# Kernel tuning notes

Hardware: AMD Instinct MI355X
Metric: run time of the kernel (lower is better)

The kernel has to match this reference:

```python
import jax, jax.numpy as jnp
import numpy as np

D_MODEL, HEADS, D_FF = 1024, 16, 4096
D_K = D_MODEL // HEADS
EPS = 1e-5


def layer_norm(x, g, b):
    mu = jnp.mean(x, axis=-1, keepdims=True)
    var = jnp.mean((x - mu) ** 2, axis=-1, keepdims=True)
    return (x - mu) * jax.lax.rsqrt(var + EPS) * g + b


def setup_inputs() -> dict:
    key = jax.random.key(0)
    ks = jax.random.split(key, 16)
    B, S = 2, 2048
    s = 0.02
    return {
        "src": jax.random.normal(ks[0], (B, S, D_MODEL), jnp.float32),
        "corr": jax.random.normal(ks[1], (B, S, S), jnp.float32),
        "pos": jax.random.normal(ks[2], (B, S, D_MODEL), jnp.float32),
        "Wq": jax.random.normal(ks[3], (D_MODEL, D_MODEL), jnp.float32) * s,
        "bq": jnp.zeros((D_MODEL,), jnp.float32),
        "Wk": jax.random.normal(ks[4], (D_MODEL, D_MODEL), jnp.float32) * s,
        "bk": jnp.zeros((D_MODEL,), jnp.float32),
        "Wv": jax.random.normal(ks[5], (D_MODEL, D_MODEL), jnp.float32) * s,
        "bv": jnp.zeros((D_MODEL,), jnp.float32),
        "Wo": jax.random.normal(ks[6], (D_MODEL, D_MODEL), jnp.float32) * s,
        "bo": jnp.zeros((D_MODEL,), jnp.float32),
        "W1": jax.random.normal(ks[7], (D_MODEL, D_FF), jnp.float32) * s,
        "b1": jnp.zeros((D_FF,), jnp.float32),
        "W2": jax.random.normal(ks[8], (D_FF, D_MODEL), jnp.float32) * s,
        "b2": jnp.zeros((D_MODEL,), jnp.float32),
        "g1": jnp.ones((D_MODEL,), jnp.float32),
        "be1": jnp.zeros((D_MODEL,), jnp.float32),
        "g2": jnp.ones((D_MODEL,), jnp.float32),
        "be2": jnp.zeros((D_MODEL,), jnp.float32),
    }


def reference(src, corr, pos, Wq, bq, Wk, bk, Wv, bv, Wo, bo, W1, b1, W2, b2, g1, be1, g2, be2):
    B, S, _ = src.shape
    qk_in = src + pos  # with_pos_embed for q and k; value uses raw src
    # QKV projections -> [B, H, S, d_k]
    def split_heads(x):
        return x.reshape(B, S, HEADS, D_K).transpose(0, 2, 1, 3)
    q = split_heads(qk_in @ Wq + bq)
    k = split_heads(qk_in @ Wk + bk)
    v = split_heads(src @ Wv + bv)
    # scores [B, H, S, S] with additive correlation bias before softmax
    scores = jnp.einsum("bhqd,bhkd->bhqk", q, k) / jnp.sqrt(jnp.float32(D_K))
    scores = scores + corr[:, None, :, :]
    attn = jax.nn.softmax(scores, axis=-1)
    ctx = jnp.einsum("bhqk,bhkd->bhqd", attn, v)
    concat = ctx.transpose(0, 2, 1, 3).reshape(B, S, D_MODEL)
    attn_out = concat @ Wo + bo
    # post-norm residual blocks (dropout = identity in eval)
    x = layer_norm(src + attn_out, g1, be1)
    ffn = jax.nn.relu(x @ W1 + b1) @ W2 + b2
    x = layer_norm(x + ffn, g2, be2)
    return x
```

## Files before the change

### kernel.cpp

```cpp
#include <hip/hip_runtime.h>
#include <hip/hip_bf16.h>

#define S_LEN  2048
#define BATCH  2
#define DMODEL 1024
#define NHEAD  16
#define DHEAD  64
#define DFF    4096
#define NTOK   (BATCH * S_LEN)
#define QKVLD  3072
#define NSPLIT 2

typedef __attribute__((ext_vector_type(8))) short short8;
typedef __attribute__((ext_vector_type(4))) short short4v;
typedef __attribute__((ext_vector_type(4))) float f32x4;

__device__ __forceinline__ short f2bs(float f) {
  __hip_bfloat16 h = __float2bfloat16(f);
  short s;
  __builtin_memcpy(&s, &h, sizeof(short));
  return s;
}

__device__ __forceinline__ float bs2f(short s) {
  unsigned u = ((unsigned)(unsigned short)s) << 16;
  float f;
  __builtin_memcpy(&f, &u, sizeof(float));
  return f;
}

__device__ __forceinline__ f32x4 mfma16(short8 a, short8 b, f32x4 c) {
  return __builtin_amdgcn_mfma_f32_16x16x32_bf16(a, b, c, 0, 0, 0);
}

__device__ __forceinline__ void load_lds16(const short* g, short* l) {
  __builtin_amdgcn_global_load_lds(
      (const __attribute__((address_space(1))) void*)g,
      (__attribute__((address_space(3))) void*)l, 16, 0, 0);
}

__global__ void prep_static(
    const float* __restrict__ Wq, const float* __restrict__ Wk,
    const float* __restrict__ Wv, const float* __restrict__ Wo,
    const float* __restrict__ W1, const float* __restrict__ W2,
    const float* __restrict__ bq, const float* __restrict__ bk,
    const float* __restrict__ bv,
    short* __restrict__ WqkvT, short* __restrict__ WoT,
    short* __restrict__ W1T, short* __restrict__ W2T,
    float* __restrict__ bqkv) {
  const int gid = blockIdx.x;
  const int tx = threadIdx.x, ty = threadIdx.y;

  if (gid >= 12288) {
    const int i = (gid - 12288) * 256 + ty * 32 + tx;
    float v;
    if (i < DMODEL) v = bq[i] * 0.125f;
    else if (i < 2 * DMODEL) v = bk[i - DMODEL];
    else v = bv[i - 2 * DMODEL];
    bqkv[i] = v;
    return;
  }

  const float* in;
  short* out;
  int R, C, t;
  float scale = 1.0f;
  if (gid < 4096) {
    t = gid & 1023;
    R = C = 1024;
    if (gid < 1024)      { in = Wq; out = WqkvT;                 scale = 0.125f; }
    else if (gid < 2048) { in = Wk; out = WqkvT + 1024 * 1024; }
    else if (gid < 3072) { in = Wv; out = WqkvT + 2 * 1024 * 1024; }
    else                 { in = Wo; out = WoT; }
  } else if (gid < 8192) {
    t = gid - 4096; in = W1; out = W1T; R = 1024; C = 4096;
  } else {
    t = gid - 8192; in = W2; out = W2T; R = 4096; C = 1024;
  }
  const int tpr = C >> 5;
  const int c0 = (t % tpr) * 32, r0 = (t / tpr) * 32;

  __shared__ float tile[32][33];
#pragma unroll
  for (int i = 0; i < 32; i += 8)
    tile[ty + i][tx] = in[(size_t)(r0 + ty + i) * C + c0 + tx];
  __syncthreads();
#pragma unroll
  for (int i = 0; i < 32; i += 8)
    out[(size_t)(c0 + ty + i) * R + r0 + tx] = f2bs(tile[tx][ty + i] * scale);
}

__global__ void prep_inputs(const float* __restrict__ src, const float* __restrict__ pos,
                            const float* __restrict__ corr,
                            short* __restrict__ qkb, short* __restrict__ srcb,
                            short* __restrict__ corrb) {
  const int gid = blockIdx.x;
  if (gid < 4096) {
    const int i = gid * 1024 + threadIdx.x * 4;
    float4 s = *(const float4*)(src + i);
    float4 p = *(const float4*)(pos + i);
    short4v q4 = {f2bs(s.x + p.x), f2bs(s.y + p.y), f2bs(s.z + p.z), f2bs(s.w + p.w)};
    short4v s4 = {f2bs(s.x), f2bs(s.y), f2bs(s.z), f2bs(s.w)};
    *(short4v*)(qkb + i) = q4;
    *(short4v*)(srcb + i) = s4;
  } else {
    const size_t i = ((size_t)(gid - 4096)) * 1024 + threadIdx.x * 4;
    float4 c = *(const float4*)(corr + i);
    short4v o = {f2bs(c.x), f2bs(c.y), f2bs(c.z), f2bs(c.w)};
    *(short4v*)(corrb + i) = o;
  }
}

__global__ __launch_bounds__(256) void transpose_bf16(
    const short* __restrict__ in, short* __restrict__ out, int R, int LDin) {
  __shared__ __attribute__((aligned(16))) short tile[64][72];
  const int c0 = blockIdx.x * 64, r0 = blockIdx.y * 64;
#pragma unroll
  for (int i = 0; i < 2; i++) {
    const int idx = threadIdx.x + 256 * i;
    const int rr = idx >> 3, cc8 = (idx & 7) * 8;
    *(int4*)(&tile[rr][cc8]) = *(const int4*)(in + (size_t)(r0 + rr) * LDin + c0 + cc8);
  }
  __syncthreads();
#pragma unroll
  for (int i = 0; i < 2; i++) {
    const int idx = threadIdx.x + 256 * i;
    const int rr = idx >> 3, cc8 = (idx & 7) * 8;
    short8 v;
#pragma unroll
    for (int j = 0; j < 8; j++) v[j] = tile[cc8 + j][rr];
    *(short8*)(out + (size_t)(c0 + rr) * R + r0 + cc8) = v;
  }
}

template <int RELU, int OUT_BF16>
__global__ __launch_bounds__(256) void gemm_bt(
    const short* __restrict__ A0, const short* __restrict__ A1,
    const short* __restrict__ Bt, const float* __restrict__ bias,
    float* __restrict__ Cf, short* __restrict__ Cb,
    int M, int N, int K, int splitcol) {
  __shared__ __attribute__((aligned(16))) short As[128 * 32];
  __shared__ __attribute__((aligned(16))) short Bs[128 * 32];

  const int tid = threadIdx.x;
  const int wave = tid >> 6, lane = tid & 63;
  const int lm = lane & 15, lq = lane >> 4;
  const int row0 = blockIdx.y * 128, col0 = blockIdx.x * 128;
  const int wr = (wave >> 1) * 64, wc = (wave & 1) * 64;

  const short* A = (col0 < splitcol) ? A0 : A1;
  const short* ag = A + (size_t)(row0 + wave * 32 + (lane >> 2)) * K + (lane & 3) * 8;
  const short* bg = Bt + (size_t)(col0 + wave * 32 + (lane >> 2)) * K + (lane & 3) * 8;
  short* asl = &As[wave * 32 * 32];
  short* bsl = &Bs[wave * 32 * 32];

  f32x4 acc[4][4];
#pragma unroll
  for (int i = 0; i < 4; i++)
#pragma unroll
    for (int j = 0; j < 4; j++) acc[i][j] = (f32x4){0.f, 0.f, 0.f, 0.f};

  for (int k0 = 0; k0 < K; k0 += 32) {
    load_lds16(ag + k0, asl);
    load_lds16(ag + (size_t)16 * K + k0, asl + 16 * 32);
    load_lds16(bg + k0, bsl);
    load_lds16(bg + (size_t)16 * K + k0, bsl + 16 * 32);
    __syncthreads();

    short8 af[4], bfr[4];
#pragma unroll
    for (int i = 0; i < 4; i++)
      af[i] = *(const short8*)(&As[(wr + 16 * i + lm) * 32 + lq * 8]);
#pragma unroll
    for (int j = 0; j < 4; j++)
      bfr[j] = *(const short8*)(&Bs[(wc + 16 * j + lm) * 32 + lq * 8]);
#pragma unroll
    for (int i = 0; i < 4; i++)
#pragma unroll
      for (int j = 0; j < 4; j++) acc[i][j] = mfma16(af[i], bfr[j], acc[i][j]);
    __syncthreads();
  }

#pragma unroll
  for (int i = 0; i < 4; i++) {
#pragma unroll
    for (int j = 0; j < 4; j++) {
      const int col = col0 + wc + 16 * j + lm;
      const float bs = bias[col];
#pragma unroll
      for (int r = 0; r < 4; r++) {
        const int row = row0 + wr + 16 * i + lq * 4 + r;
        float v = acc[i][j][r] + bs;
        if (RELU) v = fmaxf(v, 0.f);
        if (OUT_BF16)
          Cb[(size_t)row * N + col] = f2bs(v);
        else
          Cf[(size_t)row * N + col] = v;
      }
    }
  }
}

__global__ __launch_bounds__(256) void gemm_bt_part(
    const short* __restrict__ A, const short* __restrict__ Bt,
    float* __restrict__ Cf, int M, int N, int K, int Kslice) {
  __shared__ __attribute__((aligned(16))) short As[128 * 32];
  __shared__ __attribute__((aligned(16))) short Bs[128 * 32];

  const int tid = threadIdx.x;
  const int wave = tid >> 6, lane = tid & 63;
  const int lm = lane & 15, lq = lane >> 4;
  const int row0 = blockIdx.y * 128, col0 = blockIdx.x * 128;
  const int kbase = blockIdx.z * Kslice;
  const int wr = (wave >> 1) * 64, wc = (wave & 1) * 64;
  Cf += (size_t)blockIdx.z * M * N;

  const short* ag = A + (size_t)(row0 + wave * 32 + (lane >> 2)) * K + (lane & 3) * 8;
  const short* bg = Bt + (size_t)(col0 + wave * 32 + (lane >> 2)) * K + (lane & 3) * 8;
  short* asl = &As[wave * 32 * 32];
  short* bsl = &Bs[wave * 32 * 32];

  f32x4 acc[4][4];
#pragma unroll
  for (int i = 0; i < 4; i++)
#pragma unroll
    for (int j = 0; j < 4; j++) acc[i][j] = (f32x4){0.f, 0.f, 0.f, 0.f};

  for (int k0 = kbase; k0 < kbase + Kslice; k0 += 32) {
    load_lds16(ag + k0, asl);
    load_lds16(ag + (size_t)16 * K + k0, asl + 16 * 32);
    load_lds16(bg + k0, bsl);
    load_lds16(bg + (size_t)16 * K + k0, bsl + 16 * 32);
    __syncthreads();

    short8 af[4], bfr[4];
#pragma unroll
    for (int i = 0; i < 4; i++)
      af[i] = *(const short8*)(&As[(wr + 16 * i + lm) * 32 + lq * 8]);
#pragma unroll
    for (int j = 0; j < 4; j++)
      bfr[j] = *(const short8*)(&Bs[(wc + 16 * j + lm) * 32 + lq * 8]);
#pragma unroll
    for (int i = 0; i < 4; i++)
#pragma unroll
      for (int j = 0; j < 4; j++) acc[i][j] = mfma16(af[i], bfr[j], acc[i][j]);
    __syncthreads();
  }

#pragma unroll
  for (int i = 0; i < 4; i++) {
#pragma unroll
    for (int j = 0; j < 4; j++) {
      const int col = col0 + wc + 16 * j + lm;
#pragma unroll
      for (int r = 0; r < 4; r++) {
        const int row = row0 + wr + 16 * i + lq * 4 + r;
        Cf[(size_t)row * N + col] = acc[i][j][r];
      }
    }
  }
}

__global__ __launch_bounds__(256, 8) void attn_kernel(
    const short* __restrict__ QKV,
    const short* __restrict__ VT,
    const short* __restrict__ corrb,
    float* __restrict__ Op,
    float* __restrict__ lp) {
  const int h = blockIdx.x, qtile = blockIdx.y;
  const int b = blockIdx.z >> 1, split = blockIdx.z & 1;
  const int koff = split * (S_LEN / NSPLIT);
  const int tid = threadIdx.x;
  const int wave = tid >> 6, lane = tid & 63;
  const int lm = lane & 15, lq = lane >> 4;
  const int qb = qtile * 64 + wave * 16;
  const int fx = lm & 7;
  const int fy = (lm >> 1) & 3;

  __shared__ __attribute__((aligned(16))) short Ks[32 * 64];
  __shared__ __attribute__((aligned(16))) short Vs[64 * 32];
  __shared__ __attribute__((aligned(16))) short Ps[4 * 16 * 32];

  const short* q0 = QKV + (size_t)(b * S_LEN + qb + lm) * QKVLD + h * DHEAD;
  const short8 qA0 = *(const short8*)(q0 + lq * 8);
  const short8 qA1 = *(const short8*)(q0 + lq * 8 + 32);

  f32x4 oA[4];
#pragma unroll
  for (int t = 0; t < 4; t++) oA[t] = (f32x4){0.f, 0.f, 0.f, 0.f};
  f32x4 lacc = (f32x4){0.f, 0.f, 0.f, 0.f};

  const short* c0 = corrb + (size_t)(b * S_LEN + qb + lm) * S_LEN;

  const int krow = tid >> 3, ku = tid & 7;
  short* kdst = &Ks[krow * 64 + ((ku ^ (krow & 7)) * 8)];
  const short* kgp = QKV + (size_t)(b * S_LEN + koff + krow) * QKVLD + DMODEL +
                     h * DHEAD + ku * 8;
  const int vrow = tid >> 2, vu = tid & 3;
  short* vdst = &Vs[vrow * 32 + ((vu ^ ((vrow >> 1) & 3)) * 8)];
  const short* vgp = VT + (size_t)(h * DHEAD + vrow) * NTOK + b * S_LEN + koff + vu * 8;

  for (int kt = koff; kt < koff + S_LEN / NSPLIT; kt += 32) {
    *(int4*)kdst = *(const int4*)kgp;
    *(int4*)vdst = *(const int4*)vgp;
    kgp += (size_t)32 * QKVLD;
    vgp += 32;
    __syncthreads();

    f32x4 sv[2];
    __builtin_amdgcn_s_setprio(1);
#pragma unroll
    for (int t = 0; t < 2; t++) {
      const int rb = (t * 16 + lm) * 64;
      const short8 kf0 = *(const short8*)(&Ks[rb + (lq ^ fx) * 8]);
      const short8 kf1 = *(const short8*)(&Ks[rb + ((lq + 4) ^ fx) * 8]);
      f32x4 a = (f32x4){0.f, 0.f, 0.f, 0.f};
      a = mfma16(kf0, qA0, a);
      a = mfma16(kf1, qA1, a);
      sv[t] = a;
    }
    __builtin_amdgcn_s_setprio(0);

#pragma unroll
    for (int t = 0; t < 2; t++) {
      const short4v cr = *(const short4v*)(c0 + kt + t * 16 + lq * 4);
#pragma unroll
      for (int r = 0; r < 4; r++)
        sv[t][r] = __expf(sv[t][r] + bs2f(cr[r]));
      lacc += sv[t];
      short4v pA = {f2bs(sv[t][0]), f2bs(sv[t][1]), f2bs(sv[t][2]), f2bs(sv[t][3])};
      const int pu = ((2 * t + (lq >> 1)) ^ fy) * 8 + (lq & 1) * 4;
      *(short4v*)(&Ps[wave * 512 + lm * 32 + pu]) = pA;
    }

    const short8 pA0 = *(const short8*)(&Ps[wave * 512 + lm * 32 + (lq ^ fy) * 8]);
    __builtin_amdgcn_s_setprio(1);
#pragma unroll
    for (int t = 0; t < 4; t++) {
      const int vrb = (t * 16 + lm) * 32;
      const short8 vf0 = *(const short8*)(&Vs[vrb + (lq ^ fy) * 8]);
      oA[t] = mfma16(vf0, pA0, oA[t]);
    }
    __builtin_amdgcn_s_setprio(0);
    __syncthreads();
  }

  float lA = lacc[0] + lacc[1] + lacc[2] + lacc[3];
  lA += __shfl_xor(lA, 16);
  lA += __shfl_xor(lA, 32);
  if (lq == 0)
    lp[((size_t)split * NTOK + b * S_LEN + qb + lm) * NHEAD + h] = lA;
  float* opA = Op + (size_t)split * NTOK * DMODEL +
               (size_t)(b * S_LEN + qb + lm) * DMODEL + h * DHEAD;
#pragma unroll
  for (int t = 0; t < 4; t++)
    *(f32x4*)(opA + t * 16 + lq * 4) = oA[t];
}

__global__ __launch_bounds__(256) void combine_ctx(
    const float* __restrict__ Op, const float* __restrict__ lp,
    short* __restrict__ ctx) {
  const size_t idx = ((size_t)blockIdx.x * 256 + threadIdx.x) * 4;
  const int token = (int)(idx >> 10);
  const int d = (int)(idx & 1023);
  const int h = d >> 6;
  f32x4 o = (f32x4){0.f, 0.f, 0.f, 0.f};
  float l = 0.f;
#pragma unroll
  for (int s = 0; s < NSPLIT; s++) {
    o += *(const f32x4*)(Op + (size_t)s * NTOK * DMODEL + idx);
    l += lp[((size_t)s * NTOK + token) * NHEAD + h];
  }
  const float inv = 1.0f / l;
  short4v ov = {f2bs(o[0] * inv), f2bs(o[1] * inv),
                f2bs(o[2] * inv), f2bs(o[3] * inv)};
  *(short4v*)(ctx + idx) = ov;
}

__global__ __launch_bounds__(256) void residual_ln3(
    const float* __restrict__ xa, const float* __restrict__ p0,
    const float* __restrict__ p1, const float* __restrict__ bias,
    const float* __restrict__ g, const float* __restrict__ be,
    float* __restrict__ outf, short* __restrict__ outb) {
  const int row = blockIdx.x;
  const int t = threadIdx.x;
  const size_t base = (size_t)row * DMODEL + t * 4;
  float4 a = *(const float4*)(xa + base);
  f32x4 q0 = *(const f32x4*)(p0 + base);
  f32x4 q1 = *(const f32x4*)(p1 + base);
  f32x4 bb = *(const f32x4*)(bias + t * 4);
  const float v0 = a.x + q0[0] + q1[0] + bb[0];
  const float v1 = a.y + q0[1] + q1[1] + bb[1];
  const float v2 = a.z + q0[2] + q1[2] + bb[2];
  const float v3 = a.w + q0[3] + q1[3] + bb[3];
  float sum = v0 + v1 + v2 + v3;
  float sq = v0 * v0 + v1 * v1 + v2 * v2 + v3 * v3;
#pragma unroll
  for (int off = 1; off < 64; off <<= 1) {
    sum += __shfl_xor(sum, off);
    sq += __shfl_xor(sq, off);
  }
  __shared__ float ssum[4], ssq[4];
  const int wave = t >> 6;
  if ((t & 63) == 0) { ssum[wave] = sum; ssq[wave] = sq; }
  __syncthreads();
  sum = ssum[0] + ssum[1] + ssum[2] + ssum[3];
  sq = ssq[0] + ssq[1] + ssq[2] + ssq[3];
  const float mean = sum * (1.0f / DMODEL);
  const float var = sq * (1.0f / DMODEL) - mean * mean;
  const float rstd = rsqrtf(var + 1e-5f);
  float4 gv = *(const float4*)(g + t * 4);
  float4 bv = *(const float4*)(be + t * 4);
  const float o0 = (v0 - mean) * rstd * gv.x + bv.x;
  const float o1 = (v1 - mean) * rstd * gv.y + bv.y;
  const float o2 = (v2 - mean) * rstd * gv.z + bv.z;
  const float o3 = (v3 - mean) * rstd * gv.w + bv.w;
  if (outf) {
    float4 ov = {o0, o1, o2, o3};
    *(float4*)(outf + base) = ov;
  }
  if (outb) {
    short4v ob = {f2bs(o0), f2bs(o1), f2bs(o2), f2bs(o3)};
    *(short4v*)(outb + base) = ob;
  }
}

extern "C" void kernel_launch(void* const* d_in, const int* in_sizes, int n_in,
                              void* d_out, int out_size, void* d_ws, size_t ws_size,
                              hipStream_t stream) {
  const float* src = (const float*)d_in[0];
  const float* corr = (const float*)d_in[1];
  const float* pos = (const float*)d_in[2];
  const float* Wq = (const float*)d_in[3];
  const float* bq = (const float*)d_in[4];
  const float* Wk = (const float*)d_in[5];
  const float* bk = (const float*)d_in[6];
  const float* Wv = (const float*)d_in[7];
  const float* bv = (const float*)d_in[8];
  const float* Wo = (const float*)d_in[9];
  const float* bo = (const float*)d_in[10];
  const float* W1 = (const float*)d_in[11];
  const float* b1 = (const float*)d_in[12];
  const float* W2 = (const float*)d_in[13];
  const float* b2 = (const float*)d_in[14];
  const float* g1 = (const float*)d_in[15];
  const float* be1 = (const float*)d_in[16];
  const float* g2 = (const float*)d_in[17];
  const float* be2 = (const float*)d_in[18];
  float* out = (float*)d_out;

  char* ws = (char*)d_ws;
  size_t off = 0;
  auto alloc = [&](size_t bytes) {
    char* p = ws + off;
    off += (bytes + 255) & ~(size_t)255;
    return p;
  };
  short* WqkvT = (short*)alloc((size_t)QKVLD * DMODEL * 2);
  short* WoT = (short*)alloc((size_t)DMODEL * DMODEL * 2);
  short* W1T = (short*)alloc((size_t)DFF * DMODEL * 2);
  short* W2T = (short*)alloc((size_t)DMODEL * DFF * 2);
  float* bqkv = (float*)alloc((size_t)QKVLD * 4);
  short* qkb = (short*)alloc((size_t)NTOK * DMODEL * 2);
  short* srcb = (short*)alloc((size_t)NTOK * DMODEL * 2);
  short* QKVb = (short*)alloc((size_t)NTOK * QKVLD * 2);
  short* VTt = (short*)alloc((size_t)DMODEL * NTOK * 2);
  short* corrb = (short*)alloc((size_t)BATCH * S_LEN * S_LEN * 2);
  short* ctxb = (short*)alloc((size_t)NTOK * DMODEL * 2);
  float* lp = (float*)alloc((size_t)NSPLIT * NTOK * NHEAD * 4);
  float* Pp = (float*)alloc((size_t)2 * NTOK * DMODEL * 4);
  short* Hb = (short*)alloc((size_t)NTOK * DFF * 2);
  float* Op = Pp;
  float* x1f = (float*)alloc((size_t)NTOK * DMODEL * 4);
  short* x1b = (short*)alloc((size_t)NTOK * DMODEL * 2);

  prep_static<<<12300, dim3(32, 8), 0, stream>>>(
      Wq, Wk, Wv, Wo, W1, W2, bq, bk, bv, WqkvT, WoT, W1T, W2T, bqkv);

  prep_inputs<<<12288, 256, 0, stream>>>(src, pos, corr, qkb, srcb, corrb);

  gemm_bt<0, 1><<<dim3(QKVLD / 128, NTOK / 128), 256, 0, stream>>>(
      qkb, srcb, WqkvT, bqkv, nullptr, QKVb, NTOK, QKVLD, DMODEL, 2048);

  transpose_bf16<<<dim3(DMODEL / 64, NTOK / 64), 256, 0, stream>>>(
      QKVb + 2048, VTt, NTOK, QKVLD);

  attn_kernel<<<dim3(NHEAD, S_LEN / 64, BATCH * NSPLIT), 256, 0, stream>>>(
      QKVb, VTt, corrb, Op, lp);
  combine_ctx<<<(NTOK * DMODEL) / (256 * 4), 256, 0, stream>>>(Op, lp, ctxb);

  gemm_bt_part<<<dim3(DMODEL / 128, NTOK / 128, 2), 256, 0, stream>>>(
      ctxb, WoT, Pp, NTOK, DMODEL, DMODEL, DMODEL / 2);

  residual_ln3<<<NTOK, 256, 0, stream>>>(src, Pp, Pp + (size_t)NTOK * DMODEL,
                                         bo, g1, be1, x1f, x1b);

  gemm_bt<1, 1><<<dim3(DFF / 128, NTOK / 128), 256, 0, stream>>>(
      x1b, x1b, W1T, b1, nullptr, Hb, NTOK, DFF, DMODEL, 1 << 30);

  gemm_bt_part<<<dim3(DMODEL / 128, NTOK / 128, 2), 256, 0, stream>>>(
      Hb, W2T, Pp, NTOK, DMODEL, DFF, DFF / 2);

  residual_ln3<<<NTOK, 256, 0, stream>>>(x1f, Pp, Pp + (size_t)NTOK * DMODEL,
                                         b2, g2, be2, out, nullptr);
}
```

Baseline: 478.2 us.

## Use 256x256 double-buffered 8-wave GEMM and 8-wave attention blocks

Replaces the 128x128 single-buffered QKV and FFN1 GEMM with a 512-thread kernel on 256x256 tiles and 64-wide K steps. It double-buffers swizzled LDS and interleaves global-to-LDS loads with MFMA phases to hide memory latency and raise data reuse. The attention kernel also grows to 8 waves covering 128 queries, with K and V staging split between the two thread halves. The cost is larger LDS use (128 KB per GEMM block), fewer GEMM blocks (e.g. 192 for QKV), and possible occupancy or tail-effect issues.

```diff
diff --git a/kernel.cpp b/kernel.cpp
--- a/kernel.cpp
+++ b/kernel.cpp
@@ -133,72 +133,154 @@
   }
 }
 
-template <int RELU, int OUT_BF16>
-__global__ __launch_bounds__(256) void gemm_bt(
+template <int RELU>
+__global__ __launch_bounds__(512, 2) void gemm_bt8(
     const short* __restrict__ A0, const short* __restrict__ A1,
     const short* __restrict__ Bt, const float* __restrict__ bias,
-    float* __restrict__ Cf, short* __restrict__ Cb,
-    int M, int N, int K, int splitcol) {
-  __shared__ __attribute__((aligned(16))) short As[128 * 32];
-  __shared__ __attribute__((aligned(16))) short Bs[128 * 32];
+    short* __restrict__ Cb, int M, int N, int K, int splitcol) {
+  __shared__ __attribute__((aligned(16))) short As[2][256 * 64];
+  __shared__ __attribute__((aligned(16))) short Bs[2][256 * 64];
 
   const int tid = threadIdx.x;
   const int wave = tid >> 6, lane = tid & 63;
   const int lm = lane & 15, lq = lane >> 4;
-  const int row0 = blockIdx.y * 128, col0 = blockIdx.x * 128;
-  const int wr = (wave >> 1) * 64, wc = (wave & 1) * 64;
-
+  const int wm = wave >> 2, wn = wave & 3;
+  const int row0 = blockIdx.y * 256, col0 = blockIdx.x * 256;
   const short* A = (col0 < splitcol) ? A0 : A1;
-  const short* ag = A + (size_t)(row0 + wave * 32 + (lane >> 2)) * K + (lane & 3) * 8;
-  const short* bg = Bt + (size_t)(col0 + wave * 32 + (lane >> 2)) * K + (lane & 3) * 8;
-  short* asl = &As[wave * 32 * 32];
-  short* bsl = &Bs[wave * 32 * 32];
-
-  f32x4 acc[4][4];
-#pragma unroll
-  for (int i = 0; i < 4; i++)
-#pragma unroll
-    for (int j = 0; j < 4; j++) acc[i][j] = (f32x4){0.f, 0.f, 0.f, 0.f};
-
-  for (int k0 = 0; k0 < K; k0 += 32) {
-    load_lds16(ag + k0, asl);
-    load_lds16(ag + (size_t)16 * K + k0, asl + 16 * 32);
-    load_lds16(bg + k0, bsl);
-    load_lds16(bg + (size_t)16 * K + k0, bsl + 16 * 32);
-    __syncthreads();
-
-    short8 af[4], bfr[4];
-#pragma unroll
-    for (int i = 0; i < 4; i++)
-      af[i] = *(const short8*)(&As[(wr + 16 * i + lm) * 32 + lq * 8]);
-#pragma unroll
-    for (int j = 0; j < 4; j++)
-      bfr[j] = *(const short8*)(&Bs[(wc + 16 * j + lm) * 32 + lq * 8]);
-#pragma unroll
-    for (int i = 0; i < 4; i++)
-#pragma unroll
-      for (int j = 0; j < 4; j++) acc[i][j] = mfma16(af[i], bfr[j], acc[i][j]);
-    __syncthreads();
-  }
-
-#pragma unroll
-  for (int i = 0; i < 4; i++) {
-#pragma unroll
-    for (int j = 0; j < 4; j++) {
-      const int col = col0 + wc + 16 * j + lm;
-      const float bs = bias[col];
-#pragma unroll
-      for (int r = 0; r < 4; r++) {
-        const int row = row0 + wr + 16 * i + lq * 4 + r;
-        float v = acc[i][j][r] + bs;
-        if (RELU) v = fmaxf(v, 0.f);
-        if (OUT_BF16)
-          Cb[(size_t)row * N + col] = f2bs(v);
-        else
-          Cf[(size_t)row * N + col] = v;
+
+  const int srow = tid >> 3;
+  const int lu = ((tid & 7) ^ (srow & 7)) * 8;
+
+#define STG(DSTHALF, SRC, LD, TR, KT) do {                                     \
+    const short* _s = (SRC) + (size_t)((TR) + srow) * (LD) +                   \
+                      (size_t)(KT) * 64 + lu;                                  \
+    load_lds16(_s, (DSTHALF) + wave * 512);                                    \
+    load_lds16(_s + (size_t)64 * (LD), (DSTHALF) + 4096 + wave * 512);         \
+  } while (0)
+
+  const int fk = lm & 7;
+  const int u0 = (lq ^ fk) * 8, u1 = ((4 + lq) ^ fk) * 8;
+  const int arow = (wm * 64 + lm) * 64;
+  const int brow = (wn * 32 + lm) * 64;
+
+  f32x4 acc[2][4][2][2];
+#pragma unroll
+  for (int a = 0; a < 2; a++)
+#pragma unroll
+    for (int i = 0; i < 4; i++)
+#pragma unroll
+      for (int b = 0; b < 2; b++)
+#pragma unroll
+        for (int j = 0; j < 2; j++) acc[a][i][b][j] = (f32x4){0.f, 0.f, 0.f, 0.f};
+
+  short8 af[4][2], bf0[2][2], bf1[2][2];
+
+  const int NT = K >> 6;
+  STG(&As[0][0],    A,  K, row0,       0);
+  STG(&Bs[0][0],    Bt, K, col0,       0);
+  STG(&As[0][8192], A,  K, row0 + 128, 0);
+  STG(&Bs[0][8192], Bt, K, col0 + 128, 0);
+  STG(&As[1][0],    A,  K, row0,       1);
+  STG(&Bs[1][0],    Bt, K, col0,       1);
+  asm volatile("s_waitcnt vmcnt(4)" ::: "memory");
+  __builtin_amdgcn_s_barrier();
+
+  for (int t = 0; t < NT; ++t) {
+    const int cur = t & 1, nxt = cur ^ 1;
+    const int t1 = (t + 1 < NT) ? t + 1 : NT - 1;
+    const int t2 = (t + 2 < NT) ? t + 2 : NT - 1;
+    const short* Ac = As[cur];
+    const short* Bc = Bs[cur];
+
+    STG(&As[nxt][8192], A, K, row0 + 128, t1);
+#pragma unroll
+    for (int i = 0; i < 4; i++) {
+      af[i][0] = *(const short8*)(&Ac[arow + i * 1024 + u0]);
+      af[i][1] = *(const short8*)(&Ac[arow + i * 1024 + u1]);
+    }
+#pragma unroll
+    for (int j = 0; j < 2; j++) {
+      bf0[j][0] = *(const short8*)(&Bc[brow + j * 1024 + u0]);
+      bf0[j][1] = *(const short8*)(&Bc[brow + j * 1024 + u1]);
+    }
+    __builtin_amdgcn_s_setprio(1);
+#pragma unroll
+    for (int i = 0; i < 4; i++)
+#pragma unroll
+      for (int j = 0; j < 2; j++) {
+        acc[0][i][0][j] = mfma16(af[i][0], bf0[j][0], acc[0][i][0][j]);
+        acc[0][i][0][j] = mfma16(af[i][1], bf0[j][1], acc[0][i][0][j]);
       }
-    }
-  }
+    __builtin_amdgcn_s_setprio(0);
+    __builtin_amdgcn_s_barrier();
+
+    STG(&Bs[nxt][8192], Bt, K, col0 + 128, t1);
+#pragma unroll
+    for (int j = 0; j < 2; j++) {
+      bf1[j][0] = *(const short8*)(&Bc[8192 + brow + j * 1024 + u0]);
+      bf1[j][1] = *(const short8*)(&Bc[8192 + brow + j * 1024 + u1]);
+    }
+    __builtin_amdgcn_s_setprio(1);
+#pragma unroll
+    for (int i = 0; i < 4; i++)
+#pragma unroll
+      for (int j = 0; j < 2; j++) {
+        acc[0][i][1][j] = mfma16(af[i][0], bf1[j][0], acc[0][i][1][j]);
+        acc[0][i][1][j] = mfma16(af[i][1], bf1[j][1], acc[0][i][1][j]);
+      }
+    __builtin_amdgcn_s_setprio(0);
+    __builtin_amdgcn_s_barrier();
+
+    STG(&As[cur][0], A, K, row0, t2);
+#pragma unroll
+    for (int i = 0; i < 4; i++) {
+      af[i][0] = *(const short8*)(&Ac[8192 + arow + i * 1024 + u0]);
+      af[i][1] = *(const short8*)(&Ac[8192 + arow + i * 1024 + u1]);
+    }
+    __builtin_amdgcn_s_setprio(1);
+#pragma unroll
+    for (int i = 0; i < 4; i++)
+#pragma unroll
+      for (int j = 0; j < 2; j++) {
+        acc[1][i][0][j] = mfma16(af[i][0], bf0[j][0], acc[1][i][0][j]);
+        acc[1][i][0][j] = mfma16(af[i][1], bf0[j][1], acc[1][i][0][j]);
+      }
+    __builtin_amdgcn_s_setprio(0);
+    __builtin_amdgcn_s_barrier();
+
+    STG(&Bs[cur][0], Bt, K, col0, t2);
+    __builtin_amdgcn_s_setprio(1);
+#pragma unroll
+    for (int i = 0; i < 4; i++)
+#pragma unroll
+      for (int j = 0; j < 2; j++) {
+        acc[1][i][1][j] = mfma16(af[i][0], bf1[j][0], acc[1][i][1][j]);
+        acc[1][i][1][j] = mfma16(af[i][1], bf1[j][1], acc[1][i][1][j]);
+      }
+    __builtin_amdgcn_s_setprio(0);
+    asm volatile("s_waitcnt vmcnt(4)" ::: "memory");
+    __builtin_amdgcn_s_barrier();
+  }
+#undef STG
+
+#pragma unroll
+  for (int a = 0; a < 2; a++)
+#pragma unroll
+    for (int i = 0; i < 4; i++)
+#pragma unroll
+      for (int b = 0; b < 2; b++)
+#pragma unroll
+        for (int j = 0; j < 2; j++) {
+          const int col = col0 + b * 128 + wn * 32 + j * 16 + lm;
+          const float bsv = bias[col];
+#pragma unroll
+          for (int r = 0; r < 4; r++) {
+            const int row = row0 + a * 128 + wm * 64 + i * 16 + lq * 4 + r;
+            float v = acc[a][i][b][j][r] + bsv;
+            if (RELU) v = fmaxf(v, 0.f);
+            Cb[(size_t)row * N + col] = f2bs(v);
+          }
+        }
 }
 
 __global__ __launch_bounds__(256) void gemm_bt_part(
@@ -261,7 +343,7 @@
   }
 }
 
-__global__ __launch_bounds__(256, 8) void attn_kernel(
+__global__ __launch_bounds__(512, 8) void attn_kernel(
     const short* __restrict__ QKV,
     const short* __restrict__ VT,
     const short* __restrict__ corrb,
@@ -273,13 +355,13 @@
   const int tid = threadIdx.x;
   const int wave = tid >> 6, lane = tid & 63;
   const int lm = lane & 15, lq = lane >> 4;
-  const int qb = qtile * 64 + wave * 16;
+  const int qb = qtile * 128 + wave * 16;
   const int fx = lm & 7;
   const int fy = (lm >> 1) & 3;
 
   __shared__ __attribute__((aligned(16))) short Ks[32 * 64];
   __shared__ __attribute__((aligned(16))) short Vs[64 * 32];
-  __shared__ __attribute__((aligned(16))) short Ps[4 * 16 * 32];
+  __shared__ __attribute__((aligned(16))) short Ps[8 * 16 * 32];
 
   const short* q0 = QKV + (size_t)(b * S_LEN + qb + lm) * QKVLD + h * DHEAD;
   const short8 qA0 = *(const short8*)(q0 + lq * 8);
@@ -292,19 +374,26 @@
 
   const short* c0 = corrb + (size_t)(b * S_LEN + qb + lm) * S_LEN;
 
-  const int krow = tid >> 3, ku = tid & 7;
-  short* kdst = &Ks[krow * 64 + ((ku ^ (krow & 7)) * 8)];
-  const short* kgp = QKV + (size_t)(b * S_LEN + koff + krow) * QKVLD + DMODEL +
-                     h * DHEAD + ku * 8;
-  const int vrow = tid >> 2, vu = tid & 3;
-  short* vdst = &Vs[vrow * 32 + ((vu ^ ((vrow >> 1) & 3)) * 8)];
-  const short* vgp = VT + (size_t)(h * DHEAD + vrow) * NTOK + b * S_LEN + koff + vu * 8;
+  const int st = tid & 255;
+  const bool isK = tid < 256;
+  short* sdst;
+  const short* sgp;
+  size_t sstep;
+  if (isK) {
+    const int krow = st >> 3, ku = st & 7;
+    sdst = &Ks[krow * 64 + ((ku ^ (krow & 7)) * 8)];
+    sgp = QKV + (size_t)(b * S_LEN + koff + krow) * QKVLD + DMODEL + h * DHEAD + ku * 8;
+    sstep = (size_t)32 * QKVLD;
+  } else {
+    const int vrow = st >> 2, vu = st & 3;
+    sdst = &Vs[vrow * 32 + ((vu ^ ((vrow >> 1) & 3)) * 8)];
+    sgp = VT + (size_t)(h * DHEAD + vrow) * NTOK + b * S_LEN + koff + vu * 8;
+    sstep = 32;
+  }
 
   for (int kt = koff; kt < koff + S_LEN / NSPLIT; kt += 32) {
-    *(int4*)kdst = *(const int4*)kgp;
-    *(int4*)vdst = *(const int4*)vgp;
-    kgp += (size_t)32 * QKVLD;
-    vgp += 32;
+    *(int4*)sdst = *(const int4*)sgp;
+    sgp += sstep;
     __syncthreads();
 
     f32x4 sv[2];
@@ -479,13 +568,13 @@
 
   prep_inputs<<<12288, 256, 0, stream>>>(src, pos, corr, qkb, srcb, corrb);
 
-  gemm_bt<0, 1><<<dim3(QKVLD / 128, NTOK / 128), 256, 0, stream>>>(
-      qkb, srcb, WqkvT, bqkv, nullptr, QKVb, NTOK, QKVLD, DMODEL, 2048);
+  gemm_bt8<0><<<dim3(QKVLD / 256, NTOK / 256), 512, 0, stream>>>(
+      qkb, srcb, WqkvT, bqkv, QKVb, NTOK, QKVLD, DMODEL, 2048);
 
   transpose_bf16<<<dim3(DMODEL / 64, NTOK / 64), 256, 0, stream>>>(
       QKVb + 2048, VTt, NTOK, QKVLD);
 
-  attn_kernel<<<dim3(NHEAD, S_LEN / 64, BATCH * NSPLIT), 256, 0, stream>>>(
+  attn_kernel<<<dim3(NHEAD, S_LEN / 128, BATCH * NSPLIT), 512, 0, stream>>>(
       QKVb, VTt, corrb, Op, lp);
   combine_ctx<<<(NTOK * DMODEL) / (256 * 4), 256, 0, stream>>>(Op, lp, ctxb);
 
@@ -495,8 +584,8 @@
   residual_ln3<<<NTOK, 256, 0, stream>>>(src, Pp, Pp + (size_t)NTOK * DMODEL,
                                          bo, g1, be1, x1f, x1b);
 
-  gemm_bt<1, 1><<<dim3(DFF / 128, NTOK / 128), 256, 0, stream>>>(
-      x1b, x1b, W1T, b1, nullptr, Hb, NTOK, DFF, DMODEL, 1 << 30);
+  gemm_bt8<1><<<dim3(DFF / 256, NTOK / 256), 512, 0, stream>>>(
+      x1b, x1b, W1T, b1, Hb, NTOK, DFF, DMODEL, 1 << 30);
 
   gemm_bt_part<<<dim3(DMODEL / 128, NTOK / 128, 2), 256, 0, stream>>>(
       Hb, W2T, Pp, NTOK, DMODEL, DFF, DFF / 2);
```

Measured after the change: 449.4 us. 1.06x faster.
